# Optimization experiments

Hardware: AMD Instinct MI355X
Metric: run time of the kernel (lower is better)

Reference implementation:

```python
import jax, jax.numpy as jnp
import numpy as np

HIER = [1, 9, 90, 900, 18000]   # hierchy_struc = get_HTS_strc(...).get_pred_loc()
N = sum(HIER)                    # total time series = attention batch dim
L = len(HIER)                    # levelcount = attention sequence dim
T = 168                          # time_step
HOR = 24                         # horizon
U = 256                          # units[0] = units[1] = units[2] = d_model
NB = 3                           # nblock
NH = 4                           # heads
DK = U // NH


def setup_inputs() -> dict:
    key = jax.random.key(0)
    ks = jax.random.split(key, 10)
    g = lambda k, shape, fan: jax.random.normal(k, shape, jnp.float32) / np.sqrt(fan)
    return {
        "x": jax.random.normal(ks[0], (N, T), jnp.float32),
        "Wl": g(ks[1], (NB, U, T), T),     # fcLSTM (bias=False)
        "Wl1": g(ks[2], (NB, U, U), U),    # fcLSTM1 (bias=False)
        "Wq": g(ks[3], (NB, U, U), U),
        "bq": jnp.zeros((NB, U), jnp.float32),
        "Wk": g(ks[4], (NB, U, U), U),
        "bk": jnp.zeros((NB, U), jnp.float32),
        "Wv": g(ks[5], (NB, U, U), U),
        "bv": jnp.zeros((NB, U), jnp.float32),
        "Wo": g(ks[6], (NB, U, U), U),     # linears[-1] of MultiHeadedAttention
        "bo": jnp.zeros((NB, U), jnp.float32),
        "W20": g(ks[7], (NB, T, U), U),    # fc20 (bias=False)
        "Wfc2": g(ks[8], (HOR, T), T),     # fc2 (bias=False)
        "level_ids": jnp.asarray(np.repeat(np.arange(L), HIER), jnp.int32),
    }


def reference(x, Wl, Wl1, Wq, bq, Wk, bk, Wv, bv, Wo, bo, W20, Wfc2, level_ids):
    softplus = jax.nn.softplus
    n = x.shape[0]
    # get_attmask: TS i (belonging to hierarchy level l) keeps only query row l,
    # applied POST-softmax (mask_matrix=None branch of attention()).
    qmask = jax.nn.one_hot(level_ids, L, dtype=x.dtype)            # (N, L)

    def heads(Y):  # (N, L, U) -> (N, NH, L, DK)
        return Y.reshape(n, L, NH, DK).transpose(0, 2, 1, 3)

    for b in range(NB):
        h = softplus(x @ Wl[b].T)                                  # acf(fcLSTM(x))
        h = softplus(h @ Wl1[b].T)                                 # acf(fcLSTM1(.))
        X = jnp.broadcast_to(h[:, None, :], (n, L, U))             # per-level token stream
        q = heads(X @ Wq[b].T + bq[b])
        k = heads(X @ Wk[b].T + bk[b])
        v = heads(X @ Wv[b].T + bv[b])
        scores = jnp.einsum('nhqd,nhkd->nhqk', q, k) / np.sqrt(DK)  # (N, NH, L, L)
        p = jax.nn.softmax(scores, axis=-1)
        p = p * qmask[:, None, :, None]                             # hierarchical scatter mask
        o = jnp.einsum('nhqk,nhkd->nhqd', p, v)
        o = o.transpose(0, 2, 1, 3).reshape(n, L, U)                # merge heads
        o = o @ Wo[b].T + bo[b]                                     # linears[-1]
        y = o[jnp.arange(n), level_ids]                             # own-level row per TS (N, U)
        x = x + y @ W20[b].T                                        # fc20 + residual, (N, T)
    return x @ Wfc2.T                                               # fc2 -> (N, HOR)
```

## Files before the change

kernel.cpp:

```cpp
#include <hip/hip_runtime.h>
#include <hip/hip_bf16.h>
#include <math.h>

#define N_TS   19000
#define RPB    80
#define NBLKS  238
#define T_DIM  168
#define T_PAD  192
#define U_DIM  256
#define NBLK   3
#define HOR    24

using bf16 = __hip_bfloat16;
typedef short v8s __attribute__((ext_vector_type(8)));
typedef float v4f __attribute__((ext_vector_type(4)));

__device__ __forceinline__ float softplus_f(float z) {
    return fmaxf(z, 0.0f) + __logf(1.0f + __expf(-fabsf(z)));
}
__device__ __forceinline__ unsigned pack2bf(float a, float b) {
    __hip_bfloat162 t = __float22bfloat162_rn(make_float2(a, b));
    return *(unsigned*)&t;
}
__device__ __forceinline__ short f2bf_s(float x) {
    bf16 h = __float2bfloat16(x); return *(short*)&h;
}
__device__ __forceinline__ v8s make_v8(float4 f0, float4 f1) {
    v8s r;
    r[0] = f2bf_s(f0.x); r[1] = f2bf_s(f0.y); r[2] = f2bf_s(f0.z); r[3] = f2bf_s(f0.w);
    r[4] = f2bf_s(f1.x); r[5] = f2bf_s(f1.y); r[6] = f2bf_s(f1.z); r[7] = f2bf_s(f1.w);
    return r;
}

__global__ __launch_bounds__(256) void wprep(
    const float* __restrict__ Wl, const float* __restrict__ Wl1,
    const float* __restrict__ Wv, const float* __restrict__ bv,
    const float* __restrict__ Wo, const float* __restrict__ bo,
    const float* __restrict__ W20, const float* __restrict__ Wfc2,
    bf16* __restrict__ Wlb, bf16* __restrict__ Wl1b, bf16* __restrict__ Wvob,
    bf16* __restrict__ W20b, bf16* __restrict__ Wfc2b, float* __restrict__ bvo)
{
    const int blk = blockIdx.x, j = threadIdx.x;
    if (blk < 192) {
        const int b = blk / 64, n0 = (blk % 64) * 4;
        const float* wo0 = Wo + (size_t)(b * 256 + n0 + 0) * 256;
        const float* wo1 = Wo + (size_t)(b * 256 + n0 + 1) * 256;
        const float* wo2 = Wo + (size_t)(b * 256 + n0 + 2) * 256;
        const float* wo3 = Wo + (size_t)(b * 256 + n0 + 3) * 256;
        const float* Wv_b = Wv + (size_t)b * 65536;
        float a0 = 0.f, a1 = 0.f, a2 = 0.f, a3 = 0.f;
        #pragma unroll 4
        for (int t = 0; t < 256; ++t) {
            float v = Wv_b[(size_t)t * 256 + j];
            a0 = fmaf(wo0[t], v, a0); a1 = fmaf(wo1[t], v, a1);
            a2 = fmaf(wo2[t], v, a2); a3 = fmaf(wo3[t], v, a3);
        }
        Wvob[(size_t)(b * 256 + n0 + 0) * 256 + j] = __float2bfloat16(a0);
        Wvob[(size_t)(b * 256 + n0 + 1) * 256 + j] = __float2bfloat16(a1);
        Wvob[(size_t)(b * 256 + n0 + 2) * 256 + j] = __float2bfloat16(a2);
        Wvob[(size_t)(b * 256 + n0 + 3) * 256 + j] = __float2bfloat16(a3);

        __shared__ float4 red[256];
        const float bvv = bv[b * 256 + j];
        red[j] = make_float4(wo0[j] * bvv, wo1[j] * bvv, wo2[j] * bvv, wo3[j] * bvv);
        __syncthreads();
        for (int s = 128; s > 0; s >>= 1) {
            if (j < s) {
                float4 x0 = red[j], x1 = red[j + s];
                red[j] = make_float4(x0.x + x1.x, x0.y + x1.y, x0.z + x1.z, x0.w + x1.w);
            }
            __syncthreads();
        }
        if (j == 0) {
            float4 r0 = red[0];
            bvo[b * 256 + n0 + 0] = r0.x + bo[b * 256 + n0 + 0];
            bvo[b * 256 + n0 + 1] = r0.y + bo[b * 256 + n0 + 1];
            bvo[b * 256 + n0 + 2] = r0.z + bo[b * 256 + n0 + 2];
            bvo[b * 256 + n0 + 3] = r0.w + bo[b * 256 + n0 + 3];
        }
    } else if (blk < 960) {
        const int idx = blk - 192, b = idx >> 8, r = idx & 255;
        if (j < T_PAD)
            Wlb[(size_t)(b * 256 + r) * T_PAD + j] =
                __float2bfloat16(j < T_DIM ? Wl[(size_t)(b * 256 + r) * T_DIM + j] : 0.f);
    } else if (blk < 1728) {
        const int idx = blk - 960, b = idx >> 8, r = idx & 255;
        Wl1b[(size_t)(b * 256 + r) * 256 + j] =
            __float2bfloat16(Wl1[(size_t)(b * 256 + r) * 256 + j]);
    } else if (blk < 2304) {
        const int idx = blk - 1728, b = idx / T_PAD, r = idx % T_PAD;
        W20b[(size_t)(b * T_PAD + r) * 256 + j] =
            __float2bfloat16(r < T_DIM ? W20[(size_t)(b * T_DIM + r) * 256 + j] : 0.f);
    } else {
        const int r = blk - 2304;
        if (j < T_PAD)
            Wfc2b[r * T_PAD + j] =
                __float2bfloat16((r < HOR && j < T_DIM) ? Wfc2[r * T_DIM + j] : 0.f);
    }
}

__global__ __launch_bounds__(512, 2) void fused_net(
    const bf16* __restrict__ Wlb, const bf16* __restrict__ Wl1b,
    const bf16* __restrict__ Wvob, const bf16* __restrict__ W20b,
    const bf16* __restrict__ Wfc2b, const float* __restrict__ bvo,
    const float* __restrict__ x, float* __restrict__ out)
{
    __shared__ __align__(16) bf16  hA[RPB * 256];
    __shared__ __align__(16) bf16  hB[RPB * 256];
    __shared__ __align__(16) float hX[RPB * 192];

    const int tid  = threadIdx.x;
    const int lane = tid & 63, w = tid >> 6;
    const int r16  = lane & 15, kq = lane >> 4;
    const int swz  = (r16 & 7) << 4;
    const int bm   = blockIdx.x * RPB;

    for (int u = tid; u < RPB * 48; u += 512) {
        const int r = u / 48, q = u - r * 48;
        const int gr = bm + r;
        float4 v = make_float4(0.f, 0.f, 0.f, 0.f);
        if (gr < N_TS && q < 42)
            v = *(const float4*)&x[(size_t)gr * T_DIM + 4 * q];
        *(float4*)((char*)hX + r * 768 + ((16 * q) ^ ((r & 7) << 4))) = v;
    }
    __syncthreads();

    for (int b = 0; b < NBLK; ++b) {
        {
            const bf16* W = Wlb + (size_t)b * 256 * T_PAD;
            v8s wreg[2][6];
            #pragma unroll
            for (int i = 0; i < 2; ++i)
                #pragma unroll
                for (int ks = 0; ks < 6; ++ks)
                    wreg[i][ks] = *(const v8s*)&W[(size_t)(32 * w + 16 * i + r16) * T_PAD + ks * 32 + 8 * kq];
            v4f acc[2][5] = {};
            #pragma unroll
            for (int ks = 0; ks < 6; ++ks)
                #pragma unroll
                for (int j = 0; j < 5; ++j) {
                    const char* base = (const char*)hX + (16 * j + r16) * 768;
                    const int   u0   = 128 * ks + 32 * kq;
                    float4 f0 = *(const float4*)(base + (u0 ^ swz));
                    float4 f1 = *(const float4*)(base + ((u0 + 16) ^ swz));
                    v8s bfr = make_v8(f0, f1);
                    acc[0][j] = __builtin_amdgcn_mfma_f32_16x16x32_bf16(wreg[0][ks], bfr, acc[0][j], 0, 0, 0);
                    acc[1][j] = __builtin_amdgcn_mfma_f32_16x16x32_bf16(wreg[1][ks], bfr, acc[1][j], 0, 0, 0);
                }
            #pragma unroll
            for (int i = 0; i < 2; ++i)
                #pragma unroll
                for (int j = 0; j < 5; ++j) {
                    float v0 = softplus_f(acc[i][j][0]), v1 = softplus_f(acc[i][j][1]);
                    float v2 = softplus_f(acc[i][j][2]), v3 = softplus_f(acc[i][j][3]);
                    const int c0  = 32 * w + 16 * i + 4 * kq;
                    const int off = (16 * j + r16) * 512 + ((2 * c0) ^ swz);
                    *(uint2*)((char*)hA + off) = make_uint2(pack2bf(v0, v1), pack2bf(v2, v3));
                }
        }
        __syncthreads();

        {
            const bf16* W = Wl1b + (size_t)b * 65536;
            v8s wreg[2][8];
            #pragma unroll
            for (int i = 0; i < 2; ++i)
                #pragma unroll
                for (int ks = 0; ks < 8; ++ks)
                    wreg[i][ks] = *(const v8s*)&W[(size_t)(32 * w + 16 * i + r16) * 256 + ks * 32 + 8 * kq];
            v4f acc[2][5] = {};
            #pragma unroll
            for (int ks = 0; ks < 8; ++ks)
                #pragma unroll
                for (int j = 0; j < 5; ++j) {
                    v8s bfr = *(const v8s*)((const char*)hA + (16 * j + r16) * 512 +
                                            ((64 * ks + 16 * kq) ^ swz));
                    acc[0][j] = __builtin_amdgcn_mfma_f32_16x16x32_bf16(wreg[0][ks], bfr, acc[0][j], 0, 0, 0);
                    acc[1][j] = __builtin_amdgcn_mfma_f32_16x16x32_bf16(wreg[1][ks], bfr, acc[1][j], 0, 0, 0);
                }
            #pragma unroll
            for (int i = 0; i < 2; ++i)
                #pragma unroll
                for (int j = 0; j < 5; ++j) {
                    float v0 = softplus_f(acc[i][j][0]), v1 = softplus_f(acc[i][j][1]);
                    float v2 = softplus_f(acc[i][j][2]), v3 = softplus_f(acc[i][j][3]);
                    const int c0  = 32 * w + 16 * i + 4 * kq;
                    const int off = (16 * j + r16) * 512 + ((2 * c0) ^ swz);
                    *(uint2*)((char*)hB + off) = make_uint2(pack2bf(v0, v1), pack2bf(v2, v3));
                }
        }
        __syncthreads();

        {
            const bf16* W = Wvob + (size_t)b * 65536;
            v8s wreg[2][8];
            #pragma unroll
            for (int i = 0; i < 2; ++i)
                #pragma unroll
                for (int ks = 0; ks < 8; ++ks)
                    wreg[i][ks] = *(const v8s*)&W[(size_t)(32 * w + 16 * i + r16) * 256 + ks * 32 + 8 * kq];
            v4f acc[2][5] = {};
            #pragma unroll
            for (int ks = 0; ks < 8; ++ks)
                #pragma unroll
                for (int j = 0; j < 5; ++j) {
                    v8s bfr = *(const v8s*)((const char*)hB + (16 * j + r16) * 512 +
                                            ((64 * ks + 16 * kq) ^ swz));
                    acc[0][j] = __builtin_amdgcn_mfma_f32_16x16x32_bf16(wreg[0][ks], bfr, acc[0][j], 0, 0, 0);
                    acc[1][j] = __builtin_amdgcn_mfma_f32_16x16x32_bf16(wreg[1][ks], bfr, acc[1][j], 0, 0, 0);
                }
            #pragma unroll
            for (int i = 0; i < 2; ++i) {
                const int c0b = 32 * w + 16 * i + 4 * kq;
                float4 bb = *(const float4*)&bvo[b * 256 + c0b];
                #pragma unroll
                for (int j = 0; j < 5; ++j) {
                    float v0 = acc[i][j][0] + bb.x, v1 = acc[i][j][1] + bb.y;
                    float v2 = acc[i][j][2] + bb.z, v3 = acc[i][j][3] + bb.w;
                    const int off = (16 * j + r16) * 512 + ((2 * c0b) ^ swz);
                    *(uint2*)((char*)hA + off) = make_uint2(pack2bf(v0, v1), pack2bf(v2, v3));
                }
            }
        }
        __syncthreads();

        {
            const bf16* W = W20b + (size_t)b * T_PAD * 256;
            const int ti0 = (w < 4) ? 2 * w : 8 + (w - 4);
            const int nti = (w < 4) ? 2 : 1;
            v8s wreg[2][8];
            #pragma unroll
            for (int i = 0; i < 2; ++i)
                if (i < nti)
                    #pragma unroll
                    for (int ks = 0; ks < 8; ++ks)
                        wreg[i][ks] = *(const v8s*)&W[(size_t)(16 * (ti0 + i) + r16) * 256 + ks * 32 + 8 * kq];
            v4f acc[2][5] = {};
            #pragma unroll
            for (int ks = 0; ks < 8; ++ks)
                #pragma unroll
                for (int j = 0; j < 5; ++j) {
                    v8s bfr = *(const v8s*)((const char*)hA + (16 * j + r16) * 512 +
                                            ((64 * ks + 16 * kq) ^ swz));
                    #pragma unroll
                    for (int i = 0; i < 2; ++i)
                        if (i < nti)
                            acc[i][j] = __builtin_amdgcn_mfma_f32_16x16x32_bf16(wreg[i][ks], bfr, acc[i][j], 0, 0, 0);
                }
            #pragma unroll
            for (int i = 0; i < 2; ++i)
                if (i < nti)
                    #pragma unroll
                    for (int j = 0; j < 5; ++j) {
                        const int c0 = 16 * (ti0 + i) + 4 * kq;
                        char* p = (char*)hX + (16 * j + r16) * 768 + ((4 * c0) ^ swz);
                        float4 v = *(float4*)p;
                        v.x += acc[i][j][0]; v.y += acc[i][j][1];
                        v.z += acc[i][j][2]; v.w += acc[i][j][3];
                        *(float4*)p = v;
                    }
        }
        __syncthreads();
    }

    for (int u = w; u < 10; u += 8) {
        const int t = u & 1, j = u >> 1;
        v4f acc = {};
        #pragma unroll
        for (int ks = 0; ks < 6; ++ks) {
            const char* base = (const char*)hX + (16 * j + r16) * 768;
            const int   u0   = 128 * ks + 32 * kq;
            float4 f0 = *(const float4*)(base + (u0 ^ swz));
            float4 f1 = *(const float4*)(base + ((u0 + 16) ^ swz));
            v8s xv = make_v8(f0, f1);
            v8s a  = *(const v8s*)&Wfc2b[(size_t)(16 * t + r16) * T_PAD + ks * 32 + 8 * kq];
            acc = __builtin_amdgcn_mfma_f32_16x16x32_bf16(a, xv, acc, 0, 0, 0);
        }
        const int grow = bm + 16 * j + r16;
        const int col  = 16 * t + 4 * kq;
        if (grow < N_TS && col < HOR)
            *(float4*)&out[(size_t)grow * HOR + col] =
                make_float4(acc[0], acc[1], acc[2], acc[3]);
    }
}

extern "C" void kernel_launch(void* const* d_in, const int* in_sizes, int n_in,
                              void* d_out, int out_size, void* d_ws, size_t ws_size,
                              hipStream_t stream) {
    const float* x    = (const float*)d_in[0];
    const float* Wl   = (const float*)d_in[1];
    const float* Wl1  = (const float*)d_in[2];
    const float* Wv   = (const float*)d_in[7];
    const float* bv   = (const float*)d_in[8];
    const float* Wo   = (const float*)d_in[9];
    const float* bo   = (const float*)d_in[10];
    const float* W20  = (const float*)d_in[11];
    const float* Wfc2 = (const float*)d_in[12];
    float* out = (float*)d_out;

    char* p = (char*)d_ws;
    auto carve = [&](size_t bytes) { char* q = p; p += (bytes + 255) & ~(size_t)255; return q; };
    bf16*  Wlb   = (bf16*)carve((size_t)NBLK * 256 * T_PAD * 2);
    bf16*  Wl1b  = (bf16*)carve((size_t)NBLK * 256 * 256 * 2);
    bf16*  Wvob  = (bf16*)carve((size_t)NBLK * 256 * 256 * 2);
    bf16*  W20b  = (bf16*)carve((size_t)NBLK * T_PAD * 256 * 2);
    bf16*  Wfc2b = (bf16*)carve((size_t)32 * T_PAD * 2);
    float* bvo   = (float*)carve((size_t)NBLK * 256 * 4);

    wprep<<<dim3(2336), dim3(256), 0, stream>>>(
        Wl, Wl1, Wv, bv, Wo, bo, W20, Wfc2, Wlb, Wl1b, Wvob, W20b, Wfc2b, bvo);
    fused_net<<<dim3(NBLKS), dim3(512), 0, stream>>>(
        Wlb, Wl1b, Wvob, W20b, Wfc2b, bvo, x, out);
}
```

Before: 173.8 us.

## Double-buffer weight registers to prefetch next GEMM weights during current compute

Each layer's weight fragments are now loaded into a second register bank while the current layer's MFMAs run, so global weight-load latency overlaps compute. The residual update also writes a bf16 copy of x into shared memory, which removes the per-iteration fp32-to-bf16 conversion in the first GEMM. Barriers are replaced with an LDS-only waitcnt plus s_barrier, so outstanding global prefetches are not drained at each barrier. The cost is much higher register pressure from holding 32 v8s fragments under launch_bounds(512,2), which may cause spills.

```diff
diff --git a/kernel.cpp b/kernel.cpp
--- a/kernel.cpp
+++ b/kernel.cpp
@@ -14,6 +14,11 @@
 using bf16 = __hip_bfloat16;
 typedef short v8s __attribute__((ext_vector_type(8)));
 typedef float v4f __attribute__((ext_vector_type(4)));
+
+#define MFMA(a, b, c) __builtin_amdgcn_mfma_f32_16x16x32_bf16((a), (b), (c), 0, 0, 0)
+
+#define BAR() do { asm volatile("s_waitcnt lgkmcnt(0)" ::: "memory"); \
+                   __builtin_amdgcn_s_barrier(); } while (0)
 
 __device__ __forceinline__ float softplus_f(float z) {
     return fmaxf(z, 0.0f) + __logf(1.0f + __expf(-fabsf(z)));
@@ -99,6 +104,50 @@
     }
 }
 
+template<int NKS, int NI>
+__device__ __forceinline__ void loadW(v8s (&dst)[16], const bf16* __restrict__ W,
+                                      int ld, int rowA, int rowB, int kq)
+{
+    #pragma unroll
+    for (int i = 0; i < NI; ++i) {
+        const int r = (i == 0) ? rowA : rowB;
+        #pragma unroll
+        for (int ks = 0; ks < NKS; ++ks)
+            dst[i * NKS + ks] = *(const v8s*)&W[(size_t)r * ld + ks * 32 + 8 * kq];
+    }
+}
+
+template<int NKS, bool SP, bool BIAS>
+__device__ __forceinline__ void computeH(const v8s (&wreg)[16],
+    const char* src, char* dst, const float* __restrict__ bias,
+    int w, int r16, int kq, int swz)
+{
+    v4f acc[2][5] = {};
+    #pragma unroll
+    for (int ks = 0; ks < NKS; ++ks)
+        #pragma unroll
+        for (int j = 0; j < 5; ++j) {
+            v8s bfr = *(const v8s*)(src + (16 * j + r16) * 512 + ((64 * ks + 16 * kq) ^ swz));
+            acc[0][j] = MFMA(wreg[0 * NKS + ks], bfr, acc[0][j]);
+            acc[1][j] = MFMA(wreg[1 * NKS + ks], bfr, acc[1][j]);
+        }
+    #pragma unroll
+    for (int i = 0; i < 2; ++i) {
+        const int c0 = 32 * w + 16 * i + 4 * kq;
+        float4 bb = make_float4(0.f, 0.f, 0.f, 0.f);
+        if (BIAS) bb = *(const float4*)&bias[c0];
+        #pragma unroll
+        for (int j = 0; j < 5; ++j) {
+            float v0 = acc[i][j][0], v1 = acc[i][j][1], v2 = acc[i][j][2], v3 = acc[i][j][3];
+            if (BIAS) { v0 += bb.x; v1 += bb.y; v2 += bb.z; v3 += bb.w; }
+            if (SP) { v0 = softplus_f(v0); v1 = softplus_f(v1);
+                      v2 = softplus_f(v2); v3 = softplus_f(v3); }
+            *(uint2*)(dst + (16 * j + r16) * 512 + ((2 * c0) ^ swz)) =
+                make_uint2(pack2bf(v0, v1), pack2bf(v2, v3));
+        }
+    }
+}
+
 __global__ __launch_bounds__(512, 2) void fused_net(
     const bf16* __restrict__ Wlb, const bf16* __restrict__ Wl1b,
     const bf16* __restrict__ Wvob, const bf16* __restrict__ W20b,
@@ -114,6 +163,10 @@
     const int r16  = lane & 15, kq = lane >> 4;
     const int swz  = (r16 & 7) << 4;
     const int bm   = blockIdx.x * RPB;
+
+    v8s wE[16], wO[16];
+
+    loadW<6, 2>(wE, Wlb, T_PAD, 32 * w + r16, 32 * w + 16 + r16, kq);
 
     for (int u = tid; u < RPB * 48; u += 512) {
         const int r = u / 48, q = u - r * 48;
@@ -121,53 +174,42 @@
         float4 v = make_float4(0.f, 0.f, 0.f, 0.f);
         if (gr < N_TS && q < 42)
             v = *(const float4*)&x[(size_t)gr * T_DIM + 4 * q];
-        *(float4*)((char*)hX + r * 768 + ((16 * q) ^ ((r & 7) << 4))) = v;
-    }
-    __syncthreads();
+        const int sr = (r & 7) << 4;
+        *(float4*)((char*)hX + r * 768 + ((16 * q) ^ sr)) = v;
+        *(uint2*)((char*)hB + r * 512 + ((8 * q) ^ sr)) =
+            make_uint2(pack2bf(v.x, v.y), pack2bf(v.z, v.w));
+    }
+    BAR();
 
     for (int b = 0; b < NBLK; ++b) {
+        loadW<8, 2>(wO, Wl1b + (size_t)b * 65536, 256,
+                    32 * w + r16, 32 * w + 16 + r16, kq);
+        computeH<6, true, false>(wE, (const char*)hB, (char*)hA, nullptr, w, r16, kq, swz);
+        BAR();
+
+        loadW<8, 2>(wE, Wvob + (size_t)b * 65536, 256,
+                    32 * w + r16, 32 * w + 16 + r16, kq);
+        computeH<8, true, false>(wO, (const char*)hA, (char*)hB, nullptr, w, r16, kq, swz);
+        BAR();
+
         {
-            const bf16* W = Wlb + (size_t)b * 256 * T_PAD;
-            v8s wreg[2][6];
-            #pragma unroll
-            for (int i = 0; i < 2; ++i)
-                #pragma unroll
-                for (int ks = 0; ks < 6; ++ks)
-                    wreg[i][ks] = *(const v8s*)&W[(size_t)(32 * w + 16 * i + r16) * T_PAD + ks * 32 + 8 * kq];
-            v4f acc[2][5] = {};
+            const bf16* W4 = W20b + (size_t)b * T_PAD * 256;
+            if (w < 4) loadW<8, 2>(wO, W4, 256, 16 * (2 * w) + r16, 16 * (2 * w + 1) + r16, kq);
+            else       loadW<8, 1>(wO, W4, 256, 16 * (8 + w - 4) + r16, 0, kq);
+        }
+        computeH<8, false, true>(wE, (const char*)hB, (char*)hA, bvo + b * 256, w, r16, kq, swz);
+        BAR();
+
+        if (b < NBLK - 1) {
+            loadW<6, 2>(wE, Wlb + (size_t)(b + 1) * 256 * T_PAD, T_PAD,
+                        32 * w + r16, 32 * w + 16 + r16, kq);
+        } else {
             #pragma unroll
             for (int ks = 0; ks < 6; ++ks)
-                #pragma unroll
-                for (int j = 0; j < 5; ++j) {
-                    const char* base = (const char*)hX + (16 * j + r16) * 768;
-                    const int   u0   = 128 * ks + 32 * kq;
-                    float4 f0 = *(const float4*)(base + (u0 ^ swz));
-                    float4 f1 = *(const float4*)(base + ((u0 + 16) ^ swz));
-                    v8s bfr = make_v8(f0, f1);
-                    acc[0][j] = __builtin_amdgcn_mfma_f32_16x16x32_bf16(wreg[0][ks], bfr, acc[0][j], 0, 0, 0);
-                    acc[1][j] = __builtin_amdgcn_mfma_f32_16x16x32_bf16(wreg[1][ks], bfr, acc[1][j], 0, 0, 0);
-                }
-            #pragma unroll
-            for (int i = 0; i < 2; ++i)
-                #pragma unroll
-                for (int j = 0; j < 5; ++j) {
-                    float v0 = softplus_f(acc[i][j][0]), v1 = softplus_f(acc[i][j][1]);
-                    float v2 = softplus_f(acc[i][j][2]), v3 = softplus_f(acc[i][j][3]);
-                    const int c0  = 32 * w + 16 * i + 4 * kq;
-                    const int off = (16 * j + r16) * 512 + ((2 * c0) ^ swz);
-                    *(uint2*)((char*)hA + off) = make_uint2(pack2bf(v0, v1), pack2bf(v2, v3));
-                }
-        }
-        __syncthreads();
-
+                wE[ks] = *(const v8s*)&Wfc2b[(size_t)(16 * (w & 1) + r16) * T_PAD + ks * 32 + 8 * kq];
+        }
         {
-            const bf16* W = Wl1b + (size_t)b * 65536;
-            v8s wreg[2][8];
-            #pragma unroll
-            for (int i = 0; i < 2; ++i)
-                #pragma unroll
-                for (int ks = 0; ks < 8; ++ks)
-                    wreg[i][ks] = *(const v8s*)&W[(size_t)(32 * w + 16 * i + r16) * 256 + ks * 32 + 8 * kq];
+            const int ti0 = (w < 4) ? 2 * w : 8 + (w - 4);
             v4f acc[2][5] = {};
             #pragma unroll
             for (int ks = 0; ks < 8; ++ks)
@@ -175,96 +217,31 @@
                 for (int j = 0; j < 5; ++j) {
                     v8s bfr = *(const v8s*)((const char*)hA + (16 * j + r16) * 512 +
                                             ((64 * ks + 16 * kq) ^ swz));
-                    acc[0][j] = __builtin_amdgcn_mfma_f32_16x16x32_bf16(wreg[0][ks], bfr, acc[0][j], 0, 0, 0);
-                    acc[1][j] = __builtin_amdgcn_mfma_f32_16x16x32_bf16(wreg[1][ks], bfr, acc[1][j], 0, 0, 0);
-                }
-            #pragma unroll
-            for (int i = 0; i < 2; ++i)
-                #pragma unroll
-                for (int j = 0; j < 5; ++j) {
-                    float v0 = softplus_f(acc[i][j][0]), v1 = softplus_f(acc[i][j][1]);
-                    float v2 = softplus_f(acc[i][j][2]), v3 = softplus_f(acc[i][j][3]);
-                    const int c0  = 32 * w + 16 * i + 4 * kq;
-                    const int off = (16 * j + r16) * 512 + ((2 * c0) ^ swz);
-                    *(uint2*)((char*)hB + off) = make_uint2(pack2bf(v0, v1), pack2bf(v2, v3));
-                }
-        }
-        __syncthreads();
-
-        {
-            const bf16* W = Wvob + (size_t)b * 65536;
-            v8s wreg[2][8];
-            #pragma unroll
-            for (int i = 0; i < 2; ++i)
-                #pragma unroll
-                for (int ks = 0; ks < 8; ++ks)
-                    wreg[i][ks] = *(const v8s*)&W[(size_t)(32 * w + 16 * i + r16) * 256 + ks * 32 + 8 * kq];
-            v4f acc[2][5] = {};
-            #pragma unroll
-            for (int ks = 0; ks < 8; ++ks)
-                #pragma unroll
-                for (int j = 0; j < 5; ++j) {
-                    v8s bfr = *(const v8s*)((const char*)hB + (16 * j + r16) * 512 +
-                                            ((64 * ks + 16 * kq) ^ swz));
-                    acc[0][j] = __builtin_amdgcn_mfma_f32_16x16x32_bf16(wreg[0][ks], bfr, acc[0][j], 0, 0, 0);
-                    acc[1][j] = __builtin_amdgcn_mfma_f32_16x16x32_bf16(wreg[1][ks], bfr, acc[1][j], 0, 0, 0);
+                    acc[0][j] = MFMA(wO[ks], bfr, acc[0][j]);
+                    if (w < 4) acc[1][j] = MFMA(wO[8 + ks], bfr, acc[1][j]);
                 }
             #pragma unroll
             for (int i = 0; i < 2; ++i) {
-                const int c0b = 32 * w + 16 * i + 4 * kq;
-                float4 bb = *(const float4*)&bvo[b * 256 + c0b];
+                if (i == 1 && w >= 4) continue;
+                const int c0 = 16 * (ti0 + i) + 4 * kq;
                 #pragma unroll
                 for (int j = 0; j < 5; ++j) {
-                    float v0 = acc[i][j][0] + bb.x, v1 = acc[i][j][1] + bb.y;
-                    float v2 = acc[i][j][2] + bb.z, v3 = acc[i][j][3] + bb.w;
-                    const int off = (16 * j + r16) * 512 + ((2 * c0b) ^ swz);
-                    *(uint2*)((char*)hA + off) = make_uint2(pack2bf(v0, v1), pack2bf(v2, v3));
+                    const int row = 16 * j + r16;
+                    char* pX = (char*)hX + row * 768 + ((4 * c0) ^ swz);
+                    float4 v = *(float4*)pX;
+                    v.x += acc[i][j][0]; v.y += acc[i][j][1];
+                    v.z += acc[i][j][2]; v.w += acc[i][j][3];
+                    *(float4*)pX = v;
+                    *(uint2*)((char*)hB + row * 512 + ((2 * c0) ^ swz)) =
+                        make_uint2(pack2bf(v.x, v.y), pack2bf(v.z, v.w));
                 }
             }
         }
-        __syncthreads();
-
-        {
-            const bf16* W = W20b + (size_t)b * T_PAD * 256;
-            const int ti0 = (w < 4) ? 2 * w : 8 + (w - 4);
-            const int nti = (w < 4) ? 2 : 1;
-            v8s wreg[2][8];
-            #pragma unroll
-            for (int i = 0; i < 2; ++i)
-                if (i < nti)
-                    #pragma unroll
-                    for (int ks = 0; ks < 8; ++ks)
-                        wreg[i][ks] = *(const v8s*)&W[(size_t)(16 * (ti0 + i) + r16) * 256 + ks * 32 + 8 * kq];
-            v4f acc[2][5] = {};
-            #pragma unroll
-            for (int ks = 0; ks < 8; ++ks)
-                #pragma unroll
-                for (int j = 0; j < 5; ++j) {
-                    v8s bfr = *(const v8s*)((const char*)hA + (16 * j + r16) * 512 +
-                                            ((64 * ks + 16 * kq) ^ swz));
-                    #pragma unroll
-                    for (int i = 0; i < 2; ++i)
-                        if (i < nti)
-                            acc[i][j] = __builtin_amdgcn_mfma_f32_16x16x32_bf16(wreg[i][ks], bfr, acc[i][j], 0, 0, 0);
-                }
-            #pragma unroll
-            for (int i = 0; i < 2; ++i)
-                if (i < nti)
-                    #pragma unroll
-                    for (int j = 0; j < 5; ++j) {
-                        const int c0 = 16 * (ti0 + i) + 4 * kq;
-                        char* p = (char*)hX + (16 * j + r16) * 768 + ((4 * c0) ^ swz);
-                        float4 v = *(float4*)p;
-                        v.x += acc[i][j][0]; v.y += acc[i][j][1];
-                        v.z += acc[i][j][2]; v.w += acc[i][j][3];
-                        *(float4*)p = v;
-                    }
-        }
-        __syncthreads();
+        BAR();
     }
 
     for (int u = w; u < 10; u += 8) {
-        const int t = u & 1, j = u >> 1;
+        const int j = u >> 1;
         v4f acc = {};
         #pragma unroll
         for (int ks = 0; ks < 6; ++ks) {
@@ -273,11 +250,10 @@
             float4 f0 = *(const float4*)(base + (u0 ^ swz));
             float4 f1 = *(const float4*)(base + ((u0 + 16) ^ swz));
             v8s xv = make_v8(f0, f1);
-            v8s a  = *(const v8s*)&Wfc2b[(size_t)(16 * t + r16) * T_PAD + ks * 32 + 8 * kq];
-            acc = __builtin_amdgcn_mfma_f32_16x16x32_bf16(a, xv, acc, 0, 0, 0);
+            acc = MFMA(wE[ks], xv, acc);
         }
         const int grow = bm + 16 * j + r16;
-        const int col  = 16 * t + 4 * kq;
+        const int col  = 16 * (u & 1) + 4 * kq;
         if (grow < N_TS && col < HOR)
             *(float4*)&out[(size_t)grow * HOR + col] =
                 make_float4(acc[0], acc[1], acc[2], acc[3]);
```

After: 167.8 us. -3.4%, faster.
